# Performance work log

Hardware: AMD Instinct MI355X
Metric: run time of the kernel (lower is better)

## Reference

```python
import jax, jax.numpy as jnp
import numpy as np
from jax import lax

VOC = 32000; H = 512; T = 256; B = 64; L = 2; MAXLEN = 32; SOS = 1


def setup_inputs() -> dict:
    key = jax.random.key(0)
    ks = jax.random.split(key, 20)
    s = 1.0 / np.sqrt(H)
    u = lambda k, shape: jax.random.uniform(k, shape, jnp.float32, -s, s)
    inp = {}
    inp["input"] = jax.random.randint(ks[0], (T, B), 0, VOC)
    inp["emb_enc"] = jax.random.normal(ks[1], (VOC, H), jnp.float32) * 0.1
    inp["emb_dec"] = jax.random.normal(ks[2], (VOC, H), jnp.float32) * 0.1
    # GRU weights, torch layout: W_ih (3H, in), W_hh (3H, H), biases (3H,); stacked over layers
    inp["enc_Wih"] = u(ks[3], (L, 3 * H, H)); inp["enc_Whh"] = u(ks[4], (L, 3 * H, H))
    inp["enc_bih"] = u(ks[5], (L, 3 * H));   inp["enc_bhh"] = u(ks[6], (L, 3 * H))
    inp["dec_Wih"] = u(ks[7], (L, 3 * H, H)); inp["dec_Whh"] = u(ks[8], (L, 3 * H, H))
    inp["dec_bih"] = u(ks[9], (L, 3 * H));   inp["dec_bhh"] = u(ks[10], (L, 3 * H))
    inp["attn_W"] = u(ks[11], (T, (L + 1) * H)); inp["attn_b"] = u(ks[12], (T,))
    inp["comb_W"] = u(ks[13], (H, 2 * H));       inp["comb_b"] = u(ks[14], (H,))
    inp["avg_W"] = u(ks[15], (1, H))   # dueling value head, no bias
    inp["adv_W"] = u(ks[16], (VOC, H)) # dueling advantage head, no bias
    return inp


def _gru_cell(x, h, Wih, Whh, bih, bhh):
    gi = x @ Wih.T + bih
    gh = h @ Whh.T + bhh
    ir, iz, in_ = jnp.split(gi, 3, axis=-1)
    hr, hz, hn = jnp.split(gh, 3, axis=-1)
    r = jax.nn.sigmoid(ir + hr)
    z = jax.nn.sigmoid(iz + hz)
    n = jnp.tanh(in_ + r * hn)
    return (1.0 - z) * n + z * h


def _gru_step(x, h, Wih, Whh, bih, bhh):
    # x: (B,H), h: (L,B,H) -> new h (L,B,H), top-layer output (B,H)
    hs = []
    for l in range(L):
        hl = _gru_cell(x, h[l], Wih[l], Whh[l], bih[l], bhh[l])
        hs.append(hl)
        x = hl
    return jnp.stack(hs), x


def _forward(input, emb_enc, emb_dec, enc_Wih, enc_Whh, enc_bih, enc_bhh,
             dec_Wih, dec_Whh, dec_bih, dec_bhh, attn_W, attn_b,
             comb_W, comb_b, avg_W, adv_W):
    # ----- encoder -----
    emb = jax.nn.relu(emb_enc[input])  # (T,B,H)
    h0 = jnp.zeros((L, B, H), jnp.float32)

    def enc_step(h, x):
        h2, top = _gru_step(x, h, enc_Wih, enc_Whh, enc_bih, enc_bhh)
        return h2, top

    states, gru_out = lax.scan(enc_step, h0, emb)  # gru_out: (T,B,H)

    def dec_step(carry, _):
        h, word = carry
        e = jax.nn.relu(emb_dec[word])                       # (B,H)
        sv = jnp.reshape(h, (B, L * H))                      # matches torch .view(-1,1,L*H)
        a = jax.nn.relu(jnp.concatenate([e, sv], -1) @ attn_W.T + attn_b)  # (B,T)
        applied = jnp.einsum('bt,tbh->bh', a, gru_out)       # (B,H)
        comb = jax.nn.relu(jnp.concatenate([e, applied], -1) @ comb_W.T + comb_b)
        h2, top = _gru_step(comb, h, dec_Wih, dec_Whh, dec_bih, dec_bhh)
        values = top @ avg_W.T + top @ adv_W.T               # (B,1)+(B,VOC) -> (B,VOC)
        word2 = jnp.argmax(values, axis=-1)
        q = jnp.take_along_axis(values, word2[:, None], axis=-1)[:, 0]
        return (h2, word2), (top, q)

    word0 = jnp.full((B,), SOS, dtype=jnp.int32)
    _, (tops, qs) = lax.scan(dec_step, (states, word0), None, length=MAXLEN)
    sentences = tops[:, None]  # (MAXLEN,1,B,H) mirrors stacking (1,B,H) rnn_outs
    return sentences, qs       # qs: (MAXLEN,B)


def reference(input, emb_enc, emb_dec, enc_Wih, enc_Whh, enc_bih, enc_bhh,
              dec_Wih, dec_Whh, dec_bih, dec_bhh, attn_W, attn_b,
              comb_W, comb_b, avg_W, adv_W):
    return _forward(input, emb_enc, emb_dec, enc_Wih, enc_Whh, enc_bih, enc_bhh,
                    dec_Wih, dec_Whh, dec_bih, dec_bhh, attn_W, attn_b,
                    comb_W, comb_b, avg_W, adv_W)
```

## Files before the change

### kernel.cpp

```cpp
#include <hip/hip_runtime.h>
#include <math.h>

#define VOCN 32000
#define HN 512
#define TN 256
#define BN 64
#define MAXLENN 32
#define SOSW 1

#define WS_FLAG     0
#define WS_REL      8192
#define WS_H        8448
#define WS_CELLS    (WS_H + 131072)
#define WS_AVG      (WS_CELLS + 4096)
#define WS_A        (WS_AVG + 64)
#define WS_APPLIED  (WS_A + 16384)
#define WS_COMB     (WS_APPLIED + 32768)
#define WS_GRUOUT   (WS_COMB + 32768)
#define WS_ZERO_BYTES ((WS_CELLS + 4096) * 4)

typedef float f4 __attribute__((ext_vector_type(4)));

__device__ __forceinline__ f4 ld4(const float* p) { return *(const f4*)p; }
__device__ __forceinline__ float dot4(f4 a, f4 b, float acc) {
  acc = fmaf(a.x, b.x, acc); acc = fmaf(a.y, b.y, acc);
  acc = fmaf(a.z, b.z, acc); acc = fmaf(a.w, b.w, acc); return acc;
}
__device__ __forceinline__ f4 relu4(f4 v) {
  v.x = fmaxf(v.x, 0.f); v.y = fmaxf(v.y, 0.f);
  v.z = fmaxf(v.z, 0.f); v.w = fmaxf(v.w, 0.f); return v;
}
__device__ __forceinline__ float sigmoidf_(float x) { return 1.f / (1.f + expf(-x)); }

__device__ __forceinline__ float ldcg(const float* p) {
  float v;
  asm volatile("global_load_dword %0, %1, off sc0 sc1\n\ts_waitcnt vmcnt(0)"
               : "=&v"(v) : "v"(p) : "memory");
  return v;
}
__device__ __forceinline__ void stcg(float* p, float v) {
  asm volatile("global_store_dword %0, %1, off sc0 sc1" :: "v"(p), "v"(v) : "memory");
}
__device__ __forceinline__ void ldcg_b4(const float* p0, const float* p1,
                                        const float* p2, const float* p3,
                                        f4& v0, f4& v1, f4& v2, f4& v3) {
  asm volatile(
      "global_load_dwordx4 %0, %4, off sc0 sc1\n\t"
      "global_load_dwordx4 %1, %5, off sc0 sc1\n\t"
      "global_load_dwordx4 %2, %6, off sc0 sc1\n\t"
      "global_load_dwordx4 %3, %7, off sc0 sc1\n\t"
      "s_waitcnt vmcnt(0)"
      : "=&v"(v0), "=&v"(v1), "=&v"(v2), "=&v"(v3)
      : "v"(p0), "v"(p1), "v"(p2), "v"(p3)
      : "memory");
}
__device__ __forceinline__ void ldcg_b8(const float* p0, const float* p1,
    const float* p2, const float* p3, const float* p4, const float* p5,
    const float* p6, const float* p7,
    f4& v0, f4& v1, f4& v2, f4& v3, f4& v4, f4& v5, f4& v6, f4& v7) {
  asm volatile(
      "global_load_dwordx4 %0, %8, off sc0 sc1\n\t"
      "global_load_dwordx4 %1, %9, off sc0 sc1\n\t"
      "global_load_dwordx4 %2, %10, off sc0 sc1\n\t"
      "global_load_dwordx4 %3, %11, off sc0 sc1\n\t"
      "global_load_dwordx4 %4, %12, off sc0 sc1\n\t"
      "global_load_dwordx4 %5, %13, off sc0 sc1\n\t"
      "global_load_dwordx4 %6, %14, off sc0 sc1\n\t"
      "global_load_dwordx4 %7, %15, off sc0 sc1\n\t"
      "s_waitcnt vmcnt(0)"
      : "=&v"(v0), "=&v"(v1), "=&v"(v2), "=&v"(v3),
        "=&v"(v4), "=&v"(v5), "=&v"(v6), "=&v"(v7)
      : "v"(p0), "v"(p1), "v"(p2), "v"(p3), "v"(p4), "v"(p5), "v"(p6), "v"(p7)
      : "memory");
}
__device__ __forceinline__ void ldcg_row8(const float* p, f4 (&v)[8]) {
  asm volatile(
      "global_load_dwordx4 %0, %8, off sc0 sc1\n\t"
      "global_load_dwordx4 %1, %8, off offset:16 sc0 sc1\n\t"
      "global_load_dwordx4 %2, %8, off offset:32 sc0 sc1\n\t"
      "global_load_dwordx4 %3, %8, off offset:48 sc0 sc1\n\t"
      "global_load_dwordx4 %4, %8, off offset:64 sc0 sc1\n\t"
      "global_load_dwordx4 %5, %8, off offset:80 sc0 sc1\n\t"
      "global_load_dwordx4 %6, %8, off offset:96 sc0 sc1\n\t"
      "global_load_dwordx4 %7, %8, off offset:112 sc0 sc1\n\t"
      "s_waitcnt vmcnt(0)"
      : "=&v"(v[0]), "=&v"(v[1]), "=&v"(v[2]), "=&v"(v[3]),
        "=&v"(v[4]), "=&v"(v[5]), "=&v"(v[6]), "=&v"(v[7])
      : "v"(p)
      : "memory");
}

__device__ __forceinline__ void grid_barrier(int* wsi, int gen) {
  asm volatile("s_waitcnt vmcnt(0) lgkmcnt(0)" ::: "memory");
  __syncthreads();
  const int bid = blockIdx.x;
  const int tid = threadIdx.x;
  if (bid == 0) {
    if (tid == 0)
      __hip_atomic_store(wsi + WS_FLAG, gen, __ATOMIC_RELAXED, __HIP_MEMORY_SCOPE_AGENT);
    int* fp = wsi + WS_FLAG + (tid & 255) * 32;
    for (;;) {
      int v = gen;
      if (tid < 256)
        v = __hip_atomic_load(fp, __ATOMIC_RELAXED, __HIP_MEMORY_SCOPE_AGENT);
      if (__syncthreads_and(v >= gen)) break;
      __builtin_amdgcn_s_sleep(2);
    }
    if (tid < 8)
      __hip_atomic_store(wsi + WS_REL + tid * 16, gen, __ATOMIC_RELAXED, __HIP_MEMORY_SCOPE_AGENT);
    __syncthreads();
  } else {
    if (tid == 0) {
      __hip_atomic_store(wsi + WS_FLAG + bid * 32, gen, __ATOMIC_RELAXED, __HIP_MEMORY_SCOPE_AGENT);
      int* rp = wsi + WS_REL + (bid & 7) * 16;
      while (__hip_atomic_load(rp, __ATOMIC_RELAXED, __HIP_MEMORY_SCOPE_AGENT) < gen)
        __builtin_amdgcn_s_sleep(2);
    }
    __syncthreads();
  }
}

__device__ __forceinline__ unsigned ord_enc(float v) {
  unsigned u = __float_as_uint(v);
  return (u & 0x80000000u) ? ~u : (u | 0x80000000u);
}
__device__ __forceinline__ float ord_dec(unsigned k32) {
  unsigned u = (k32 & 0x80000000u) ? (k32 ^ 0x80000000u) : ~k32;
  return __uint_as_float(u);
}
__device__ __forceinline__ int decode_word(const unsigned long long* cell) {
  unsigned long long key = __hip_atomic_load(cell, __ATOMIC_RELAXED,
                                             __HIP_MEMORY_SCOPE_AGENT);
  int wb = (int)(0xFFFFFFFFu - (unsigned)(key & 0xFFFFFFFFull));
  return wb < 0 ? 0 : (wb > VOCN - 1 ? VOCN - 1 : wb);
}

__device__ __forceinline__ void gru_phase(
    const float* __restrict__ x_base, const int* __restrict__ tok,
    const float* __restrict__ h_rows,
    const float* __restrict__ Wih, const float* __restrict__ Whh,
    const float* __restrict__ bih, const float* __restrict__ bhh,
    float* __restrict__ h_out, float* __restrict__ aux_out,
    int jg, float* lds)
{
  const int tid = threadIdx.x;
  const int tid2 = tid & 255;
  const int bg = tid >> 8;
  f4* x4l = (f4*)lds + (bg << 11);
  f4* h4l = x4l + 1024;

  const float* xp[4]; const float* hp[4]; int loff[4];
#pragma unroll
  for (int i = 0; i < 4; ++i) {
    int tau = tid2 + (i << 8);
    int b = tau >> 5;
    int kq = tau & 31;
    int gb = bg * 32 + b;
    const float* xr = tok ? (x_base + (size_t)tok[gb] * HN) : (x_base + (size_t)gb * HN);
    xp[i] = xr + (kq << 2);
    hp[i] = h_rows + (size_t)gb * HN + (kq << 2);
    loff[i] = (b << 5) + (kq ^ (b & 7));
  }
  const bool cachedx = (tok != nullptr);
  f4 pxv[4], phv[4];
  if (cachedx) {
#pragma unroll
    for (int i = 0; i < 4; ++i) pxv[i] = ld4(xp[i]);
    ldcg_b4(hp[0], hp[1], hp[2], hp[3], phv[0], phv[1], phv[2], phv[3]);
  } else {
    ldcg_b8(xp[0], xp[1], xp[2], xp[3], hp[0], hp[1], hp[2], hp[3],
            pxv[0], pxv[1], pxv[2], pxv[3], phv[0], phv[1], phv[2], phv[3]);
  }

  const int bl = tid2 & 31;
  const int jl = tid2 >> 5;
  const int j = (jg << 3) + jl;
  const float* wi0 = Wih + (size_t)j * HN;
  const float* wi1 = Wih + (size_t)(512 + j) * HN;
  const float* wi2 = Wih + (size_t)(1024 + j) * HN;
  const float* wh0 = Whh + (size_t)j * HN;
  const float* wh1 = Whh + (size_t)(512 + j) * HN;
  const float* wh2 = Whh + (size_t)(1024 + j) * HN;
  float ax0 = 0.f, ax1 = 0.f, ax2 = 0.f, ah0 = 0.f, ah1 = 0.f, ah2 = 0.f;
  const int rdbase = bl << 5;
  const int rdx = bl & 7;

#pragma unroll 1
  for (int ch = 0; ch < 4; ++ch) {
    __syncthreads();
#pragma unroll
    for (int i = 0; i < 4; ++i) {
      x4l[loff[i]] = cachedx ? relu4(pxv[i]) : pxv[i];
      h4l[loff[i]] = phv[i];
    }
    __syncthreads();
    if (ch < 3) {
      const int off = (ch + 1) * 128;
      if (cachedx) {
#pragma unroll
        for (int i = 0; i < 4; ++i) pxv[i] = ld4(xp[i] + off);
        ldcg_b4(hp[0] + off, hp[1] + off, hp[2] + off, hp[3] + off,
                phv[0], phv[1], phv[2], phv[3]);
      } else {
        ldcg_b8(xp[0] + off, xp[1] + off, xp[2] + off, xp[3] + off,
                hp[0] + off, hp[1] + off, hp[2] + off, hp[3] + off,
                pxv[0], pxv[1], pxv[2], pxv[3], phv[0], phv[1], phv[2], phv[3]);
      }
    }
    const int k0 = ch << 7;
#pragma unroll 4
    for (int kq = 0; kq < 32; ++kq) {
      f4 xv = x4l[rdbase + (kq ^ rdx)];
      f4 hv = h4l[rdbase + (kq ^ rdx)];
      const int kk = k0 + (kq << 2);
      ax0 = dot4(xv, ld4(wi0 + kk), ax0);
      ah0 = dot4(hv, ld4(wh0 + kk), ah0);
      ax1 = dot4(xv, ld4(wi1 + kk), ax1);
      ah1 = dot4(hv, ld4(wh1 + kk), ah1);
      ax2 = dot4(xv, ld4(wi2 + kk), ax2);
      ah2 = dot4(hv, ld4(wh2 + kk), ah2);
    }
  }
  const int gb = bg * 32 + bl;
  const float hold = ldcg(h_rows + (size_t)gb * HN + j);
  const float r = sigmoidf_(ax0 + bih[j] + ah0 + bhh[j]);
  const float z = sigmoidf_(ax1 + bih[512 + j] + ah1 + bhh[512 + j]);
  const float n = tanhf(ax2 + bih[1024 + j] + r * (ah2 + bhh[1024 + j]));
  const float hv = (1.f - z) * n + z * hold;
  stcg(h_out + (size_t)gb * HN + j, hv);
  if (aux_out) stcg(aux_out + (size_t)gb * HN + j, hv);
}

__device__ __forceinline__ void d1_attn(
    const float* __restrict__ emb_dec, const unsigned long long* __restrict__ cells,
    int s, const float* __restrict__ hflat, const float* __restrict__ attn_W,
    const float* __restrict__ attn_b, float* __restrict__ a_buf,
    const float* __restrict__ avg_buf, float* __restrict__ qs_base,
    int bid, float* lds)
{
  const int tid = threadIdx.x;
  const int b = tid & 63, q = tid >> 6;
  int* wlds = (int*)(lds + 576);
  if (s > 0 && tid < 64)
    wlds[tid] = decode_word(cells + (size_t)(s - 1) * 64 + tid);
  if (s > 0 && bid == 0 && tid < 64) {
    unsigned long long key = __hip_atomic_load(cells + (size_t)(s - 1) * 64 + tid,
                                               __ATOMIC_RELAXED, __HIP_MEMORY_SCOPE_AGENT);
    qs_base[(size_t)(s - 1) * BN + tid] = ord_dec((unsigned)(key >> 32)) + ldcg(avg_buf + tid);
  }
  __syncthreads();
  const int wb = (s == 0) ? SOSW : wlds[b];
  const float* er = emb_dec + (size_t)wb * HN;
  const float* hr = hflat + b * 1024;
  const float* wr = attn_W + (size_t)bid * 1536;
  float acc = 0.f;
  const int kbeg = q * 192, kend = kbeg + 192;
  int k = kbeg;
  const int kc = (kend < 512) ? kend : 512;
  for (; k < kc; k += 4)
    acc = dot4(relu4(ld4(er + k)), ld4(wr + k), acc);
  if (k < 512) k = 512;
  for (; k < kend; k += 32) {
    f4 hv[8]; ldcg_row8(hr + (k - 512), hv);
#pragma unroll
    for (int jq = 0; jq < 8; ++jq)
      acc = dot4(hv[jq], ld4(wr + k + (jq << 2)), acc);
  }
  __syncthreads();
  lds[(b << 3) + q] = acc;
  __syncthreads();
  if (tid < 64) {
    float v = 0.f;
#pragma unroll
    for (int i = 0; i < 8; ++i) v += lds[(tid << 3) + i];
    v += attn_b[bid];
    stcg(a_buf + tid * 256 + bid, fmaxf(v, 0.f));
  }
}

__device__ __forceinline__ void d2_applied(const float* __restrict__ a_buf,
    const float* __restrict__ gru_out, float* __restrict__ applied, int bid, float* lds)
{
  const int tid = threadIdx.x;
  const int b = bid & 63, hc = bid >> 6;
  f4* al4 = (f4*)lds;
  float* al = lds;
  float* red = lds + 256;
  if (tid < 64) {
    f4 av;
    const float* p = a_buf + b * 256 + (tid << 2);
    asm volatile("global_load_dwordx4 %0, %1, off sc0 sc1\n\ts_waitcnt vmcnt(0)"
                 : "=&v"(av) : "v"(p) : "memory");
    al4[tid] = av;
  }
  __syncthreads();
  const int hl = tid & 127, th = tid >> 7;
  const int hh = (hc << 7) + hl;
  const float* gp = gru_out + (size_t)b * HN + hh;
  float acc = 0.f;
  const int t0 = th << 6;
#pragma unroll 4
  for (int t = t0; t < t0 + 64; ++t)
    acc = fmaf(al[t], gp[(size_t)t * (BN * HN)], acc);
  red[tid] = acc;
  __syncthreads();
  if (tid < 128)
    stcg(applied + (size_t)b * HN + (hc << 7) + tid,
         red[tid] + red[tid + 128] + red[tid + 256] + red[tid + 384]);
}

__device__ __forceinline__ void d3_comb(const float* __restrict__ emb_dec,
    const unsigned long long* __restrict__ cells, int s,
    const float* __restrict__ applied, const float* __restrict__ comb_W,
    const float* __restrict__ comb_b, float* __restrict__ comb, int bid, float* lds)
{
  const int tid = threadIdx.x;
  const int b = tid & 63, q = tid >> 6;
  int* wlds = (int*)(lds + 1088);
  if (s > 0 && tid < 64)
    wlds[tid] = decode_word(cells + (size_t)(s - 1) * 64 + tid);
  __syncthreads();
  const int wb = (s == 0) ? SOSW : wlds[b];
  const float* er = emb_dec + (size_t)wb * HN;
  const float* apr = applied + (size_t)b * HN;
  const int col0 = bid << 1;
  const float* w0 = comb_W + (size_t)col0 * 1024;
  const float* w1 = w0 + 1024;
  float a0 = 0.f, a1 = 0.f;
  const int kb = q << 7;
  if (q < 4) {
    for (int k = kb; k < kb + 128; k += 4) {
      f4 e = relu4(ld4(er + k));
      a0 = dot4(e, ld4(w0 + k), a0);
      a1 = dot4(e, ld4(w1 + k), a1);
    }
  } else {
#pragma unroll 1
    for (int r = 0; r < 4; ++r) {
      f4 av[8]; ldcg_row8(apr + (kb - 512) + (r << 5), av);
#pragma unroll
      for (int jq = 0; jq < 8; ++jq) {
        a0 = dot4(av[jq], ld4(w0 + kb + (r << 5) + (jq << 2)), a0);
        a1 = dot4(av[jq], ld4(w1 + kb + (r << 5) + (jq << 2)), a1);
      }
    }
  }
  __syncthreads();
  lds[(b << 3) + q] = a0;
  lds[512 + (b << 3) + q] = a1;
  __syncthreads();
  if (tid < 128) {
    const int cc = tid >> 6, b2 = tid & 63;
    const float* base = lds + cc * 512;
    float v = 0.f;
#pragma unroll
    for (int i = 0; i < 8; ++i) v += base[(b2 << 3) + i];
    v += comb_b[col0 + cc];
    stcg(comb + (size_t)b2 * HN + col0 + cc, fmaxf(v, 0.f));
  }
}

__device__ __forceinline__ void d6_values(const float* __restrict__ top,
    const float* __restrict__ adv_W, const float* __restrict__ avg_W,
    unsigned long long* __restrict__ cellsS, float* __restrict__ avg_buf,
    int bid, float* lds)
{
  const int tid = threadIdx.x;
  const int c0 = bid * 125;
  f4* tl = (f4*)lds;
  f4* wl = ((f4*)lds) + 2048;

  const float* tp[4]; int loff[4];
#pragma unroll
  for (int i = 0; i < 4; ++i) {
    int tau = tid + (i << 9);
    int b = tau >> 5, kq = tau & 31;
    tp[i] = top + b * HN + (kq << 2);
    loff[i] = (b << 5) + (kq ^ (b & 7));
  }
  f4 pv[4];
  ldcg_b4(tp[0], tp[1], tp[2], tp[3], pv[0], pv[1], pv[2], pv[3]);

  const int rp = tid >> 4;
  const int co = tid & 15;
  const int r0 = rp << 1;
  float acc0[8], acc1[8];
#pragma unroll
  for (int i = 0; i < 8; ++i) { acc0[i] = 0.f; acc1[i] = 0.f; }
  float avgacc = 0.f;

#pragma unroll 1
  for (int ch = 0; ch < 4; ++ch) {
    __syncthreads();
#pragma unroll
    for (int i = 0; i < 4; ++i) tl[loff[i]] = pv[i];
    __syncthreads();
    if (ch < 3) {
      const int off = (ch + 1) * 128;
      ldcg_b4(tp[0] + off, tp[1] + off, tp[2] + off, tp[3] + off,
              pv[0], pv[1], pv[2], pv[3]);
    }
    if (bid == 0 && tid < 64) {
#pragma unroll 4
      for (int kq = 0; kq < 32; ++kq)
        avgacc = dot4(tl[(tid << 5) + (kq ^ (tid & 7))],
                      ld4(avg_W + (ch << 7) + (kq << 2)), avgacc);
    }
#pragma unroll 1
    for (int w = 0; w < 2; ++w) {
#pragma unroll
      for (int r = 0; r < 4; ++r) {
        const int qq = tid + (r << 9);
        const int cl = qq >> 4, kql = qq & 15;
        int c = c0 + cl; if (c > VOCN - 1) c = VOCN - 1;
        wl[(cl << 4) + (kql ^ ((cl >> 3) & 7))] =
            ld4(adv_W + (size_t)c * HN + (ch << 7) + (w << 6) + (kql << 2));
      }
      __syncthreads();
      const int kqb = w << 4;
#pragma unroll 2
      for (int kql = 0; kql < 16; ++kql) {
        const int kq = kqb + kql;
        f4 t0 = tl[(r0 << 5) + (kq ^ (r0 & 7))];
        f4 t1 = tl[((r0 + 1) << 5) + (kq ^ ((r0 + 1) & 7))];
#pragma unroll
        for (int j = 0; j < 8; ++j) {
          const int cl = (co << 3) + j;
          f4 wv = wl[(cl << 4) + (kql ^ ((cl >> 3) & 7))];
          acc0[j] = dot4(t0, wv, acc0[j]);
          acc1[j] = dot4(t1, wv, acc1[j]);
        }
      }
      __syncthreads();
    }
  }
  float bv0 = -3.4e38f, bv1 = -3.4e38f; int bi0 = 2147483647, bi1 = 2147483647;
#pragma unroll
  for (int j = 0; j < 8; ++j) {
    const int cl = (co << 3) + j;
    if (cl < 125) {
      if (acc0[j] > bv0) { bv0 = acc0[j]; bi0 = c0 + cl; }
      if (acc1[j] > bv1) { bv1 = acc1[j]; bi1 = c0 + cl; }
    }
  }
  float* sval = lds;
  int* sidx = (int*)(lds + 1024);
  sval[(r0 << 4) + co] = bv0;  sidx[(r0 << 4) + co] = bi0;
  sval[((r0 + 1) << 4) + co] = bv1;  sidx[((r0 + 1) << 4) + co] = bi1;
  __syncthreads();
  if (tid < 64) {
    float v = sval[tid << 4]; int ii = sidx[tid << 4];
#pragma unroll
    for (int h2 = 1; h2 < 16; ++h2) {
      float v2 = sval[(tid << 4) + h2]; int i2 = sidx[(tid << 4) + h2];
      if (v2 > v || (v2 == v && i2 < ii)) { v = v2; ii = i2; }
    }
    unsigned long long key = ((unsigned long long)ord_enc(v) << 32) |
                             (unsigned long long)(0xFFFFFFFFu - (unsigned)ii);
    __hip_atomic_fetch_max(cellsS + tid, key, __ATOMIC_RELAXED,
                           __HIP_MEMORY_SCOPE_AGENT);
  }
  if (bid == 0 && tid < 64) stcg(avg_buf + tid, avgacc);
}

__global__ void __launch_bounds__(512)
seq2seq_kernel(const int* __restrict__ input, const float* __restrict__ emb_enc,
               const float* __restrict__ emb_dec,
               const float* __restrict__ enc_Wih, const float* __restrict__ enc_Whh,
               const float* __restrict__ enc_bih, const float* __restrict__ enc_bhh,
               const float* __restrict__ dec_Wih, const float* __restrict__ dec_Whh,
               const float* __restrict__ dec_bih, const float* __restrict__ dec_bhh,
               const float* __restrict__ attn_W, const float* __restrict__ attn_b,
               const float* __restrict__ comb_W, const float* __restrict__ comb_b,
               const float* __restrict__ avg_W, const float* __restrict__ adv_W,
               float* __restrict__ out, float* __restrict__ ws)
{
  __shared__ float lds[16384];
  const int bid = blockIdx.x;
  int* wsi = (int*)ws;
  float* hbuf = ws + WS_H;
  unsigned long long* cells = (unsigned long long*)(ws + WS_CELLS);
  float* avg_buf = ws + WS_AVG;
  float* a_buf = ws + WS_A;
  float* applied = ws + WS_APPLIED;
  float* comb = ws + WS_COMB;
  float* gru_out = ws + WS_GRUOUT;
  float* qs_base = out + (size_t)MAXLENN * BN * HN;
  int gen = 0;

#pragma unroll 1
  for (int p = 0; p <= 256; ++p) {
    if (bid < 64) {
      if (p < 256) {
        gru_phase(emb_enc, input + p * BN,
                  hbuf + (size_t)(p & 1) * 65536,
                  enc_Wih, enc_Whh, enc_bih, enc_bhh,
                  hbuf + (size_t)((p + 1) & 1) * 65536,
                  nullptr, bid, lds);
      }
    } else if (bid < 128) {
      if (p >= 1) {
        const int t = p - 1;
        gru_phase(hbuf + (size_t)((t + 1) & 1) * 65536, nullptr,
                  hbuf + (size_t)(t & 1) * 65536 + 32768,
                  enc_Wih + 786432, enc_Whh + 786432,
                  enc_bih + 1536, enc_bhh + 1536,
                  hbuf + (size_t)((t + 1) & 1) * 65536 + 32768,
                  gru_out + (size_t)t * (BN * HN), bid - 64, lds);
      }
    }
    grid_barrier(wsi, ++gen);
  }

  __threadfence();

#pragma unroll 1
  for (int s = 0; s < 32; ++s) {
    const float* hflat = hbuf + (size_t)(s & 1) * 65536;
    float* hnew = hbuf + (size_t)((s + 1) & 1) * 65536;

    d1_attn(emb_dec, cells, s, hflat, attn_W, attn_b, a_buf, avg_buf, qs_base, bid, lds);
    grid_barrier(wsi, ++gen);

    d2_applied(a_buf, gru_out, applied, bid, lds);
    grid_barrier(wsi, ++gen);

    d3_comb(emb_dec, cells, s, applied, comb_W, comb_b, comb, bid, lds);
    grid_barrier(wsi, ++gen);

    if (bid < 64)
      gru_phase(comb, nullptr, hflat, dec_Wih, dec_Whh, dec_bih, dec_bhh,
                hnew, nullptr, bid, lds);
    grid_barrier(wsi, ++gen);

    if (bid < 64)
      gru_phase(hnew, nullptr, hflat + 32768,
                dec_Wih + 786432, dec_Whh + 786432, dec_bih + 1536, dec_bhh + 1536,
                hnew + 32768, out + (size_t)s * (BN * HN), bid, lds);
    grid_barrier(wsi, ++gen);

    d6_values(hnew + 32768, adv_W, avg_W, cells + (size_t)s * 64, avg_buf, bid, lds);
    grid_barrier(wsi, ++gen);
  }

  if (bid == 0 && threadIdx.x < 64) {
    const int tid = threadIdx.x;
    unsigned long long key = __hip_atomic_load(cells + (size_t)31 * 64 + tid,
                                               __ATOMIC_RELAXED, __HIP_MEMORY_SCOPE_AGENT);
    qs_base[(size_t)31 * BN + tid] = ord_dec((unsigned)(key >> 32)) + ldcg(avg_buf + tid);
  }
}

extern "C" void kernel_launch(void* const* d_in, const int* in_sizes, int n_in,
                              void* d_out, int out_size, void* d_ws, size_t ws_size,
                              hipStream_t stream) {
  (void)in_sizes; (void)n_in; (void)out_size; (void)ws_size;
  const int* input      = (const int*)d_in[0];
  const float* emb_enc  = (const float*)d_in[1];
  const float* emb_dec  = (const float*)d_in[2];
  const float* enc_Wih  = (const float*)d_in[3];
  const float* enc_Whh  = (const float*)d_in[4];
  const float* enc_bih  = (const float*)d_in[5];
  const float* enc_bhh  = (const float*)d_in[6];
  const float* dec_Wih  = (const float*)d_in[7];
  const float* dec_Whh  = (const float*)d_in[8];
  const float* dec_bih  = (const float*)d_in[9];
  const float* dec_bhh  = (const float*)d_in[10];
  const float* attn_W   = (const float*)d_in[11];
  const float* attn_b   = (const float*)d_in[12];
  const float* comb_W   = (const float*)d_in[13];
  const float* comb_b   = (const float*)d_in[14];
  const float* avg_W    = (const float*)d_in[15];
  const float* adv_W    = (const float*)d_in[16];
  float* out = (float*)d_out;
  float* ws  = (float*)d_ws;

  hipMemsetAsync(d_ws, 0, WS_ZERO_BYTES, stream);

  seq2seq_kernel<<<dim3(256), dim3(512), 0, stream>>>(
      input, emb_enc, emb_dec, enc_Wih, enc_Whh, enc_bih, enc_bhh,
      dec_Wih, dec_Whh, dec_bih, dec_bhh, attn_W, attn_b,
      comb_W, comb_b, avg_W, adv_W, out, ws);
}
```

Before: 21.76 ms.

## Register-prefetch adv_W tiles and split attention-apply accumulators

The vocab projection stage now prefetches the next adv_W tile into registers with nontemporal loads while the current tile is consumed from LDS, merging the chunk and half loops into one eight-phase loop with fewer barriers. The attention-apply reduction uses eight independent accumulators so more gru_out loads are in flight at once. The aim is to hide global load latency for the large weight stream, at the cost of extra registers that could reduce occupancy.

```diff
diff --git a/kernel.cpp b/kernel.cpp
--- a/kernel.cpp
+++ b/kernel.cpp
@@ -22,6 +22,9 @@
 typedef float f4 __attribute__((ext_vector_type(4)));
 
 __device__ __forceinline__ f4 ld4(const float* p) { return *(const f4*)p; }
+__device__ __forceinline__ f4 ldnt4(const float* p) {
+  return __builtin_nontemporal_load((const f4*)p);
+}
 __device__ __forceinline__ float dot4(f4 a, f4 b, float acc) {
   acc = fmaf(a.x, b.x, acc); acc = fmaf(a.y, b.y, acc);
   acc = fmaf(a.z, b.z, acc); acc = fmaf(a.w, b.w, acc); return acc;
@@ -297,12 +300,21 @@
   const int hl = tid & 127, th = tid >> 7;
   const int hh = (hc << 7) + hl;
   const float* gp = gru_out + (size_t)b * HN + hh;
-  float acc = 0.f;
+  float a0 = 0.f, a1 = 0.f, a2 = 0.f, a3 = 0.f;
+  float a4 = 0.f, a5 = 0.f, a6 = 0.f, a7 = 0.f;
   const int t0 = th << 6;
-#pragma unroll 4
-  for (int t = t0; t < t0 + 64; ++t)
-    acc = fmaf(al[t], gp[(size_t)t * (BN * HN)], acc);
-  red[tid] = acc;
+#pragma unroll 2
+  for (int t = t0; t < t0 + 64; t += 8) {
+    a0 = fmaf(al[t + 0], gp[(size_t)(t + 0) * (BN * HN)], a0);
+    a1 = fmaf(al[t + 1], gp[(size_t)(t + 1) * (BN * HN)], a1);
+    a2 = fmaf(al[t + 2], gp[(size_t)(t + 2) * (BN * HN)], a2);
+    a3 = fmaf(al[t + 3], gp[(size_t)(t + 3) * (BN * HN)], a3);
+    a4 = fmaf(al[t + 4], gp[(size_t)(t + 4) * (BN * HN)], a4);
+    a5 = fmaf(al[t + 5], gp[(size_t)(t + 5) * (BN * HN)], a5);
+    a6 = fmaf(al[t + 6], gp[(size_t)(t + 6) * (BN * HN)], a6);
+    a7 = fmaf(al[t + 7], gp[(size_t)(t + 7) * (BN * HN)], a7);
+  }
+  red[tid] = ((a0 + a1) + (a2 + a3)) + ((a4 + a5) + (a6 + a7));
   __syncthreads();
   if (tid < 128)
     stcg(applied + (size_t)b * HN + (hc << 7) + tid,
@@ -381,6 +393,21 @@
   f4 pv[4];
   ldcg_b4(tp[0], tp[1], tp[2], tp[3], pv[0], pv[1], pv[2], pv[3]);
 
+  const int kql = tid & 15;
+  const int clb = tid >> 4;
+  int cadr[4]; int wdst[4];
+#pragma unroll
+  for (int r = 0; r < 4; ++r) {
+    const int cl = clb + (r << 5);
+    int c = c0 + cl; if (c > VOCN - 1) c = VOCN - 1;
+    cadr[r] = c;
+    wdst[r] = (cl << 4) + (kql ^ ((cl >> 3) & 7));
+  }
+  f4 wv[4];
+#pragma unroll
+  for (int r = 0; r < 4; ++r)
+    wv[r] = ldnt4(adv_W + (size_t)cadr[r] * HN + (kql << 2));
+
   const int rp = tid >> 4;
   const int co = tid & 15;
   const int r0 = rp << 1;
@@ -390,50 +417,51 @@
   float avgacc = 0.f;
 
 #pragma unroll 1
-  for (int ch = 0; ch < 4; ++ch) {
+  for (int ph = 0; ph < 8; ++ph) {
+    const int ch = ph >> 1, w = ph & 1;
     __syncthreads();
-#pragma unroll
-    for (int i = 0; i < 4; ++i) tl[loff[i]] = pv[i];
+    if (w == 0) {
+#pragma unroll
+      for (int i = 0; i < 4; ++i) tl[loff[i]] = pv[i];
+    }
+#pragma unroll
+    for (int r = 0; r < 4; ++r) wl[wdst[r]] = wv[r];
     __syncthreads();
-    if (ch < 3) {
+    if (ph < 7) {
+      const int chn = (ph + 1) >> 1, wn = (ph + 1) & 1;
+      const int koff = (chn << 7) + (wn << 6) + (kql << 2);
+#pragma unroll
+      for (int r = 0; r < 4; ++r)
+        wv[r] = ldnt4(adv_W + (size_t)cadr[r] * HN + koff);
+    }
+    if (w == 0 && ch < 3) {
       const int off = (ch + 1) * 128;
       ldcg_b4(tp[0] + off, tp[1] + off, tp[2] + off, tp[3] + off,
               pv[0], pv[1], pv[2], pv[3]);
     }
-    if (bid == 0 && tid < 64) {
+    if (w == 0 && bid == 0 && tid < 64) {
 #pragma unroll 4
       for (int kq = 0; kq < 32; ++kq)
         avgacc = dot4(tl[(tid << 5) + (kq ^ (tid & 7))],
                       ld4(avg_W + (ch << 7) + (kq << 2)), avgacc);
     }
-#pragma unroll 1
-    for (int w = 0; w < 2; ++w) {
-#pragma unroll
-      for (int r = 0; r < 4; ++r) {
-        const int qq = tid + (r << 9);
-        const int cl = qq >> 4, kql = qq & 15;
-        int c = c0 + cl; if (c > VOCN - 1) c = VOCN - 1;
-        wl[(cl << 4) + (kql ^ ((cl >> 3) & 7))] =
-            ld4(adv_W + (size_t)c * HN + (ch << 7) + (w << 6) + (kql << 2));
+    const int kqb = w << 4;
+#pragma unroll 2
+    for (int kqi = 0; kqi < 16; ++kqi) {
+      const int kq = kqb + kqi;
+      f4 t0v = tl[(r0 << 5) + (kq ^ (r0 & 7))];
+      f4 t1v = tl[((r0 + 1) << 5) + (kq ^ ((r0 + 1) & 7))];
+#pragma unroll
+      for (int j = 0; j < 8; ++j) {
+        const int cl = (co << 3) + j;
+        f4 wv4 = wl[(cl << 4) + (kqi ^ ((cl >> 3) & 7))];
+        acc0[j] = dot4(t0v, wv4, acc0[j]);
+        acc1[j] = dot4(t1v, wv4, acc1[j]);
       }
-      __syncthreads();
-      const int kqb = w << 4;
-#pragma unroll 2
-      for (int kql = 0; kql < 16; ++kql) {
-        const int kq = kqb + kql;
-        f4 t0 = tl[(r0 << 5) + (kq ^ (r0 & 7))];
-        f4 t1 = tl[((r0 + 1) << 5) + (kq ^ ((r0 + 1) & 7))];
-#pragma unroll
-        for (int j = 0; j < 8; ++j) {
-          const int cl = (co << 3) + j;
-          f4 wv = wl[(cl << 4) + (kql ^ ((cl >> 3) & 7))];
-          acc0[j] = dot4(t0, wv, acc0[j]);
-          acc1[j] = dot4(t1, wv, acc1[j]);
-        }
-      }
-      __syncthreads();
-    }
-  }
+    }
+  }
+  __syncthreads();
+
   float bv0 = -3.4e38f, bv1 = -3.4e38f; int bi0 = 2147483647, bi1 = 2147483647;
 #pragma unroll
   for (int j = 0; j < 8; ++j) {
```

New measurement: 21.54 ms. About the same (-1.0%).
